# Optimization experiments

Measured on AMD Instinct MI355X. Metric: run time of the kernel, lower is better.

## Reference

```python
import jax, jax.numpy as jnp
import numpy as np

N = 1_000_000
D = 64      # input_size
O = 64      # output_size


def setup_inputs() -> dict:
    key = jax.random.key(0)
    k1, k2, k3, k4, k5 = jax.random.split(key, 5)
    x = jax.random.normal(k1, (N, D), dtype=jnp.float32)
    item_to_left_idxs = jax.random.randint(k2, (N,), 0, N, dtype=jnp.int64 if jax.config.jax_enable_x64 else jnp.int32)
    item_to_right_idxs = jax.random.randint(k3, (N,), 0, N, dtype=jnp.int64 if jax.config.jax_enable_x64 else jnp.int32)
    # nn.Linear(3*D, O): weight [O, 3*D], bias [O]
    bound = 1.0 / np.sqrt(3 * D)
    W = jax.random.uniform(k4, (O, 3 * D), dtype=jnp.float32, minval=-bound, maxval=bound)
    b = jax.random.uniform(k5, (O,), dtype=jnp.float32, minval=-bound, maxval=bound)
    return {"x": x, "item_to_left_idxs": item_to_left_idxs,
            "item_to_right_idxs": item_to_right_idxs, "W": W, "b": b}


def reference(x, item_to_left_idxs, item_to_right_idxs, W, b):
    # cat((x, x[left], x[right]), -1) @ W.T + b
    # Expressed as three smaller GEMMs on the weight slices to avoid
    # materializing the [N, 3D] concat (same math as the torch module).
    Wx, Wl, Wr = W[:, :D], W[:, D:2 * D], W[:, 2 * D:]
    out = (jnp.einsum('nd,od->no', x, Wx)
           + jnp.einsum('nd,od->no', x[item_to_left_idxs], Wl)
           + jnp.einsum('nd,od->no', x[item_to_right_idxs], Wr)
           + b)
    return out
```

## Files before the change

kernel.cpp:

```cpp
#include <hip/hip_runtime.h>


typedef __bf16 bf16x8 __attribute__((ext_vector_type(8)));
typedef float floatx4 __attribute__((ext_vector_type(4)));

#define D 64
#define O 64
#define K3 192

__device__ __forceinline__ void issue_gather(floatx4 (&v)[12], const float* __restrict__ x,
                                             int item, int li, int ri, int quad) {
    const float* px = x + (size_t)item * D + quad * 8;
    const float* pl = x + (size_t)li   * D + quad * 8;
    const float* pr = x + (size_t)ri   * D + quad * 8;
    v[0]  = *(const floatx4*)(px);      v[1]  = *(const floatx4*)(px + 4);
    v[2]  = *(const floatx4*)(px + 32); v[3]  = *(const floatx4*)(px + 36);
    v[4]  = *(const floatx4*)(pl);      v[5]  = *(const floatx4*)(pl + 4);
    v[6]  = *(const floatx4*)(pl + 32); v[7]  = *(const floatx4*)(pl + 36);
    v[8]  = *(const floatx4*)(pr);      v[9]  = *(const floatx4*)(pr + 4);
    v[10] = *(const floatx4*)(pr + 32); v[11] = *(const floatx4*)(pr + 36);
}

__device__ __forceinline__ void compute_store(const floatx4 (&v)[12],
                                              const bf16x8 (&bfrag)[6][4],
                                              const float (&bi)[4],
                                              float* __restrict__ out,
                                              int base, int col, int quad) {
    bf16x8 afrag[6];
#pragma unroll
    for (int ks = 0; ks < 6; ++ks) {
        floatx4 a0 = v[2 * ks], a1 = v[2 * ks + 1];
        bf16x8 f;
        f[0] = (__bf16)a0[0]; f[1] = (__bf16)a0[1];
        f[2] = (__bf16)a0[2]; f[3] = (__bf16)a0[3];
        f[4] = (__bf16)a1[0]; f[5] = (__bf16)a1[1];
        f[6] = (__bf16)a1[2]; f[7] = (__bf16)a1[3];
        afrag[ks] = f;
    }
    floatx4 acc[4];
#pragma unroll
    for (int ct = 0; ct < 4; ++ct)
        acc[ct] = (floatx4){bi[ct], bi[ct], bi[ct], bi[ct]};
#pragma unroll
    for (int ct = 0; ct < 4; ++ct)
#pragma unroll
        for (int ks = 0; ks < 6; ++ks)
            acc[ct] = __builtin_amdgcn_mfma_f32_16x16x32_bf16(
                afrag[ks], bfrag[ks][ct], acc[ct], 0, 0, 0);

    float* orow = out + (size_t)base * O;
#pragma unroll
    for (int ct = 0; ct < 4; ++ct)
#pragma unroll
        for (int r = 0; r < 4; ++r) {
            int m = quad * 4 + r;
            __builtin_nontemporal_store(acc[ct][r],
                                        orow + (size_t)m * O + ct * 16 + col);
        }
}

__global__ __launch_bounds__(256, 2) void polyconv_kernel(
    const float* __restrict__ x,
    const int* __restrict__ lidx,
    const int* __restrict__ ridx,
    const float* __restrict__ W,
    const float* __restrict__ bias,
    float* __restrict__ out,
    int n_tiles, int total_waves)
{
    const int lane = threadIdx.x & 63;
    const int wave_id = blockIdx.x * (blockDim.x >> 6) + (threadIdx.x >> 6);
    const int col  = lane & 15;
    const int quad = lane >> 4;

    bf16x8 bfrag[6][4];
#pragma unroll
    for (int ct = 0; ct < 4; ++ct) {
        const float* wrow = W + (size_t)(ct * 16 + col) * K3 + quad * 8;
#pragma unroll
        for (int ks = 0; ks < 6; ++ks) {
            floatx4 w0 = *(const floatx4*)(wrow + ks * 32);
            floatx4 w1 = *(const floatx4*)(wrow + ks * 32 + 4);
            bf16x8 f;
            f[0] = (__bf16)w0[0]; f[1] = (__bf16)w0[1];
            f[2] = (__bf16)w0[2]; f[3] = (__bf16)w0[3];
            f[4] = (__bf16)w1[0]; f[5] = (__bf16)w1[1];
            f[6] = (__bf16)w1[2]; f[7] = (__bf16)w1[3];
            bfrag[ks][ct] = f;
        }
    }
    float bi[4];
#pragma unroll
    for (int ct = 0; ct < 4; ++ct) bi[ct] = bias[ct * 16 + col];

    const int stride = total_waves;
    int t = wave_id;
    if (t >= n_tiles) return;

    floatx4 va[12], vb[12];
    int li_n = 0, ri_n = 0;

    {
        int item = t * 16 + col;
        int li = lidx[item], ri = ridx[item];
        issue_gather(va, x, item, li, ri, quad);
    }
    int t1 = t + stride;
    if (t1 < n_tiles) { li_n = lidx[t1 * 16 + col]; ri_n = ridx[t1 * 16 + col]; }

    while (true) {
        if (t1 < n_tiles) {
            issue_gather(vb, x, t1 * 16 + col, li_n, ri_n, quad);
            int t2 = t1 + stride;
            if (t2 < n_tiles) { li_n = lidx[t2 * 16 + col]; ri_n = ridx[t2 * 16 + col]; }
        }
        compute_store(va, bfrag, bi, out, t * 16, col, quad);
        t = t1; t1 += stride;
        if (t >= n_tiles) break;

        if (t1 < n_tiles) {
            issue_gather(va, x, t1 * 16 + col, li_n, ri_n, quad);
            int t2 = t1 + stride;
            if (t2 < n_tiles) { li_n = lidx[t2 * 16 + col]; ri_n = ridx[t2 * 16 + col]; }
        }
        compute_store(vb, bfrag, bi, out, t * 16, col, quad);
        t = t1; t1 += stride;
        if (t >= n_tiles) break;
    }
}

extern "C" void kernel_launch(void* const* d_in, const int* in_sizes, int n_in,
                              void* d_out, int out_size, void* d_ws, size_t ws_size,
                              hipStream_t stream) {
    const float* x  = (const float*)d_in[0];
    const int*   li = (const int*)d_in[1];
    const int*   ri = (const int*)d_in[2];
    const float* W  = (const float*)d_in[3];
    const float* b  = (const float*)d_in[4];
    float* out = (float*)d_out;

    const int n = in_sizes[1];
    const int n_tiles = n / 16;
    const int blocks = 512;
    const int total_waves = blocks * 4;
    polyconv_kernel<<<blocks, 256, 0, stream>>>(x, li, ri, W, b, out,
                                                n_tiles, total_waves);
}
```

Before: 516.8 us.

## Pre-convert x to bf16 in workspace and gather half-width rows

Adds a streaming pre-pass that converts x to a bf16 copy in the workspace. The main kernel then gathers 128-byte bf16 rows for self, left and right neighbours instead of 256-byte fp32 rows, cutting random-gather traffic and register pressure. The cost is an extra full read of x plus a write of the bf16 copy before the main kernel. The grid size is also raised from 512 to 1024 blocks, and the old fp32 path is kept as a fallback when no workspace is available.

```diff
diff --git a/kernel.cpp b/kernel.cpp
--- a/kernel.cpp
+++ b/kernel.cpp
@@ -8,8 +8,133 @@
 #define O 64
 #define K3 192
 
-__device__ __forceinline__ void issue_gather(floatx4 (&v)[12], const float* __restrict__ x,
-                                             int item, int li, int ri, int quad) {
+__global__ __launch_bounds__(256) void convert_x_bf16(
+    const float* __restrict__ x, __bf16* __restrict__ xb, long n8)
+{
+    long i = (long)blockIdx.x * 256 + threadIdx.x;
+    const long stride = (long)gridDim.x * 256;
+    for (; i < n8; i += stride) {
+        floatx4 a = __builtin_nontemporal_load((const floatx4*)x + 2 * i);
+        floatx4 b = __builtin_nontemporal_load((const floatx4*)x + 2 * i + 1);
+        bf16x8 f;
+        f[0] = (__bf16)a[0]; f[1] = (__bf16)a[1];
+        f[2] = (__bf16)a[2]; f[3] = (__bf16)a[3];
+        f[4] = (__bf16)b[0]; f[5] = (__bf16)b[1];
+        f[6] = (__bf16)b[2]; f[7] = (__bf16)b[3];
+        ((bf16x8*)xb)[i] = f;
+    }
+}
+
+__device__ __forceinline__ void issue_gather_bf16(bf16x8 (&v)[6],
+                                                  const __bf16* __restrict__ xb,
+                                                  int item, int li, int ri, int quad) {
+    const __bf16* px = xb + (size_t)item * D + quad * 8;
+    const __bf16* pl = xb + (size_t)li   * D + quad * 8;
+    const __bf16* pr = xb + (size_t)ri   * D + quad * 8;
+    v[0] = *(const bf16x8*)(px); v[1] = *(const bf16x8*)(px + 32);
+    v[2] = *(const bf16x8*)(pl); v[3] = *(const bf16x8*)(pl + 32);
+    v[4] = *(const bf16x8*)(pr); v[5] = *(const bf16x8*)(pr + 32);
+}
+
+__device__ __forceinline__ void compute_store_bf16(const bf16x8 (&v)[6],
+                                                   const bf16x8 (&bfrag)[6][4],
+                                                   const float (&bi)[4],
+                                                   float* __restrict__ out,
+                                                   int base, int col, int quad) {
+    floatx4 acc[4];
+#pragma unroll
+    for (int ct = 0; ct < 4; ++ct)
+        acc[ct] = (floatx4){bi[ct], bi[ct], bi[ct], bi[ct]};
+#pragma unroll
+    for (int ct = 0; ct < 4; ++ct)
+#pragma unroll
+        for (int ks = 0; ks < 6; ++ks)
+            acc[ct] = __builtin_amdgcn_mfma_f32_16x16x32_bf16(
+                v[ks], bfrag[ks][ct], acc[ct], 0, 0, 0);
+
+    float* orow = out + (size_t)base * O;
+#pragma unroll
+    for (int ct = 0; ct < 4; ++ct)
+#pragma unroll
+        for (int r = 0; r < 4; ++r) {
+            int m = quad * 4 + r;
+            __builtin_nontemporal_store(acc[ct][r],
+                                        orow + (size_t)m * O + ct * 16 + col);
+        }
+}
+
+__global__ __launch_bounds__(256, 2) void polyconv_bf16(
+    const __bf16* __restrict__ xb,
+    const int* __restrict__ lidx,
+    const int* __restrict__ ridx,
+    const float* __restrict__ W,
+    const float* __restrict__ bias,
+    float* __restrict__ out,
+    int n_tiles, int total_waves)
+{
+    const int lane = threadIdx.x & 63;
+    const int wave_id = blockIdx.x * (blockDim.x >> 6) + (threadIdx.x >> 6);
+    const int col  = lane & 15;
+    const int quad = lane >> 4;
+
+    bf16x8 bfrag[6][4];
+#pragma unroll
+    for (int ct = 0; ct < 4; ++ct) {
+        const float* wrow = W + (size_t)(ct * 16 + col) * K3 + quad * 8;
+#pragma unroll
+        for (int ks = 0; ks < 6; ++ks) {
+            floatx4 w0 = *(const floatx4*)(wrow + ks * 32);
+            floatx4 w1 = *(const floatx4*)(wrow + ks * 32 + 4);
+            bf16x8 f;
+            f[0] = (__bf16)w0[0]; f[1] = (__bf16)w0[1];
+            f[2] = (__bf16)w0[2]; f[3] = (__bf16)w0[3];
+            f[4] = (__bf16)w1[0]; f[5] = (__bf16)w1[1];
+            f[6] = (__bf16)w1[2]; f[7] = (__bf16)w1[3];
+            bfrag[ks][ct] = f;
+        }
+    }
+    float bi[4];
+#pragma unroll
+    for (int ct = 0; ct < 4; ++ct) bi[ct] = bias[ct * 16 + col];
+
+    const int stride = total_waves;
+    int t = wave_id;
+    if (t >= n_tiles) return;
+
+    bf16x8 va[6], vb[6];
+    int li_n = 0, ri_n = 0;
+
+    {
+        int item = t * 16 + col;
+        int li = lidx[item], ri = ridx[item];
+        issue_gather_bf16(va, xb, item, li, ri, quad);
+    }
+    int t1 = t + stride;
+    if (t1 < n_tiles) { li_n = lidx[t1 * 16 + col]; ri_n = ridx[t1 * 16 + col]; }
+
+    while (true) {
+        if (t1 < n_tiles) {
+            issue_gather_bf16(vb, xb, t1 * 16 + col, li_n, ri_n, quad);
+            int t2 = t1 + stride;
+            if (t2 < n_tiles) { li_n = lidx[t2 * 16 + col]; ri_n = ridx[t2 * 16 + col]; }
+        }
+        compute_store_bf16(va, bfrag, bi, out, t * 16, col, quad);
+        t = t1; t1 += stride;
+        if (t >= n_tiles) break;
+
+        if (t1 < n_tiles) {
+            issue_gather_bf16(va, xb, t1 * 16 + col, li_n, ri_n, quad);
+            int t2 = t1 + stride;
+            if (t2 < n_tiles) { li_n = lidx[t2 * 16 + col]; ri_n = ridx[t2 * 16 + col]; }
+        }
+        compute_store_bf16(vb, bfrag, bi, out, t * 16, col, quad);
+        t = t1; t1 += stride;
+        if (t >= n_tiles) break;
+    }
+}
+
+__device__ __forceinline__ void issue_gather_f32(floatx4 (&v)[12], const float* __restrict__ x,
+                                                 int item, int li, int ri, int quad) {
     const float* px = x + (size_t)item * D + quad * 8;
     const float* pl = x + (size_t)li   * D + quad * 8;
     const float* pr = x + (size_t)ri   * D + quad * 8;
@@ -21,11 +146,11 @@
     v[10] = *(const floatx4*)(pr + 32); v[11] = *(const floatx4*)(pr + 36);
 }
 
-__device__ __forceinline__ void compute_store(const floatx4 (&v)[12],
-                                              const bf16x8 (&bfrag)[6][4],
-                                              const float (&bi)[4],
-                                              float* __restrict__ out,
-                                              int base, int col, int quad) {
+__device__ __forceinline__ void compute_store_f32(const floatx4 (&v)[12],
+                                                  const bf16x8 (&bfrag)[6][4],
+                                                  const float (&bi)[4],
+                                                  float* __restrict__ out,
+                                                  int base, int col, int quad) {
     bf16x8 afrag[6];
 #pragma unroll
     for (int ks = 0; ks < 6; ++ks) {
@@ -103,27 +228,27 @@
     {
         int item = t * 16 + col;
         int li = lidx[item], ri = ridx[item];
-        issue_gather(va, x, item, li, ri, quad);
+        issue_gather_f32(va, x, item, li, ri, quad);
     }
     int t1 = t + stride;
     if (t1 < n_tiles) { li_n = lidx[t1 * 16 + col]; ri_n = ridx[t1 * 16 + col]; }
 
     while (true) {
         if (t1 < n_tiles) {
-            issue_gather(vb, x, t1 * 16 + col, li_n, ri_n, quad);
-            int t2 = t1 + stride;
-            if (t2 < n_tiles) { li_n = lidx[t2 * 16 + col]; ri_n = ridx[t2 * 16 + col]; }
-        }
-        compute_store(va, bfrag, bi, out, t * 16, col, quad);
-        t = t1; t1 += stride;
-        if (t >= n_tiles) break;
-
-        if (t1 < n_tiles) {
-            issue_gather(va, x, t1 * 16 + col, li_n, ri_n, quad);
-            int t2 = t1 + stride;
-            if (t2 < n_tiles) { li_n = lidx[t2 * 16 + col]; ri_n = ridx[t2 * 16 + col]; }
-        }
-        compute_store(vb, bfrag, bi, out, t * 16, col, quad);
+            issue_gather_f32(vb, x, t1 * 16 + col, li_n, ri_n, quad);
+            int t2 = t1 + stride;
+            if (t2 < n_tiles) { li_n = lidx[t2 * 16 + col]; ri_n = ridx[t2 * 16 + col]; }
+        }
+        compute_store_f32(va, bfrag, bi, out, t * 16, col, quad);
+        t = t1; t1 += stride;
+        if (t >= n_tiles) break;
+
+        if (t1 < n_tiles) {
+            issue_gather_f32(va, x, t1 * 16 + col, li_n, ri_n, quad);
+            int t2 = t1 + stride;
+            if (t2 < n_tiles) { li_n = lidx[t2 * 16 + col]; ri_n = ridx[t2 * 16 + col]; }
+        }
+        compute_store_f32(vb, bfrag, bi, out, t * 16, col, quad);
         t = t1; t1 += stride;
         if (t >= n_tiles) break;
     }
@@ -141,8 +266,21 @@
 
     const int n = in_sizes[1];
     const int n_tiles = n / 16;
-    const int blocks = 512;
-    const int total_waves = blocks * 4;
-    polyconv_kernel<<<blocks, 256, 0, stream>>>(x, li, ri, W, b, out,
-                                                n_tiles, total_waves);
-}
+    const size_t need = (size_t)n * D * sizeof(__bf16);
+
+    if (d_ws != nullptr && ws_size >= need) {
+        __bf16* xb = (__bf16*)d_ws;
+        const long n8 = (long)n * D / 8;
+        convert_x_bf16<<<2048, 256, 0, stream>>>(x, xb, n8);
+
+        const int blocks = 1024;
+        const int total_waves = blocks * 4;
+        polyconv_bf16<<<blocks, 256, 0, stream>>>(xb, li, ri, W, b, out,
+                                                  n_tiles, total_waves);
+    } else {
+        const int blocks = 1024;
+        const int total_waves = blocks * 4;
+        polyconv_kernel<<<blocks, 256, 0, stream>>>(x, li, ri, W, b, out,
+                                                    n_tiles, total_waves);
+    }
+}
```

After: 537.8 us. +4.1%, slower.
